# Kernel tuning notes

Measured on AMD Instinct MI355X. Metric: run time of the kernel, lower is better.

Reference implementation:

```python
import jax, jax.numpy as jnp
import numpy as np

N_IMG, M_GT, P_PROP = 16, 128, 8192
NUM_CLASSES = 80
THRESH_LO, THRESH_HI = 0.3, 0.7  # cfg.MODEL.ROI_HEADS.IOU_THRESHOLDS


def _make_boxes(key, shape, coord_scale=1000.0, wh_scale=200.0):
    k1, k2 = jax.random.split(key)
    xy = jax.random.uniform(k1, shape[:-1] + (2,)) * coord_scale
    wh = jax.random.uniform(k2, shape[:-1] + (2,)) * wh_scale + 1.0
    return jnp.concatenate([xy, xy + wh], axis=-1)  # [..., 4] = x1,y1,x2,y2


def setup_inputs() -> dict:
    key = jax.random.key(0)
    kg, kp, kc, ki = jax.random.split(key, 4)
    gt_boxes = _make_boxes(kg, (N_IMG, M_GT, 4))
    proposal_boxes = _make_boxes(kp, (N_IMG, P_PROP, 4))
    gt_classes = jax.random.randint(kc, (N_IMG, M_GT), 0, NUM_CLASSES, dtype=jnp.int32)
    gt_ignores = jax.random.randint(ki, (N_IMG, M_GT), 0, 2) > 0  # bool
    return {
        "gt_boxes": gt_boxes,
        "proposal_boxes": proposal_boxes,
        "gt_classes": gt_classes,
        "gt_ignores": gt_ignores,
    }


def _pairwise_iou(gt, pr):
    # gt: [N, M, 4], pr: [N, P, 4] -> iou [N, M, P]
    area_g = (gt[..., 2] - gt[..., 0]) * (gt[..., 3] - gt[..., 1])  # [N, M]
    area_p = (pr[..., 2] - pr[..., 0]) * (pr[..., 3] - pr[..., 1])  # [N, P]
    lt = jnp.maximum(gt[:, :, None, :2], pr[:, None, :, :2])  # [N, M, P, 2]
    rb = jnp.minimum(gt[:, :, None, 2:], pr[:, None, :, 2:])
    wh = jnp.clip(rb - lt, 0.0)
    inter = wh[..., 0] * wh[..., 1]  # [N, M, P]
    union = area_g[:, :, None] + area_p[:, None, :] - inter
    return jnp.where(inter > 0, inter / jnp.maximum(union, 1e-9), 0.0)


def reference(gt_boxes, proposal_boxes, gt_classes, gt_ignores):
    iou = _pairwise_iou(gt_boxes, proposal_boxes)  # [N, M, P]

    # Matcher: best GT per proposal + threshold labels (0=bg, -1=ignore, 1=fg)
    matched_vals = jnp.max(iou, axis=1)               # [N, P]
    matched_idxs = jnp.argmax(iou, axis=1).astype(jnp.int32)  # [N, P]
    matched_labels = jnp.where(
        matched_vals >= THRESH_HI, 1,
        jnp.where(matched_vals >= THRESH_LO, -1, 0),
    ).astype(jnp.int32)

    # gt_ignores toggling: proposals overlapping an ignored GT above high thresh -> -1
    neg_inf = jnp.float32(-1e30)
    max_ig = jnp.max(jnp.where(gt_ignores[:, :, None], iou, neg_inf), axis=1)  # [N, P]
    matched_labels = jnp.where(max_ig > THRESH_HI, -1, matched_labels)

    # _sample_proposals label assignment (full vector; random subsampling omitted)
    prop_gt_classes = jnp.take_along_axis(gt_classes, matched_idxs, axis=1)  # [N, P]
    prop_gt_classes = jnp.where(matched_labels == 0, NUM_CLASSES, prop_gt_classes)
    prop_gt_classes = jnp.where(matched_labels == -1, -1, prop_gt_classes)

    return iou, matched_idxs, matched_labels, prop_gt_classes
```

## Files before the change

kernel.cpp:

```cpp
#include <hip/hip_runtime.h>

#define N_IMG 16
#define M_GT 128
#define P_PROP 8192
#define NUM_CLASSES 80
#define THREADS 256

#define QUARTERS 4
#define MQ (M_GT / QUARTERS)
#define PPT 2
#define PBLK (THREADS * PPT)
#define NPBLK (P_PROP / PBLK)
#define NP (N_IMG * P_PROP)

__global__ __launch_bounds__(THREADS) void iou_kernel(
    const float* __restrict__ gt_boxes,
    const float* __restrict__ pr_boxes,
    const void*  __restrict__ gt_ignores,
    float* __restrict__ out,
    float* __restrict__ ws)
{
    __shared__ float4 s_box[MQ];
    __shared__ float  s_ag[MQ];
    __shared__ int    s_ign[MQ];
    __shared__ int    s_b01, s_bf;

    const int tid  = threadIdx.x;
    const int q    = blockIdx.x & 3;
    const int pblk = (blockIdx.x >> 2) & (NPBLK - 1);
    const int n    = blockIdx.x >> 6;

    if (tid == 0) { s_b01 = 0; s_bf = 0; }
    __syncthreads();
    {
        const int* w = (const int*)gt_ignores;
        int bad01 = 0, badf = 0;
        for (int i = tid; i < 512; i += THREADS) {
            int v = w[i];
            bad01 |= (v != 0) & (v != 1);
            badf  |= (v != 0) & (v != 0x3F800000);
        }
        if (bad01) atomicOr(&s_b01, 1);
        if (badf)  atomicOr(&s_bf, 1);
    }
    __syncthreads();
    const int mode = s_b01 ? (s_bf ? 1 : 2) : 0;

    if (tid < MQ) {
        const int m = q * MQ + tid;
        const float4 g = *reinterpret_cast<const float4*>(gt_boxes + ((size_t)n * M_GT + m) * 4);
        s_box[tid] = g;
        s_ag[tid]  = (g.z - g.x) * (g.w - g.y);
        int ig;
        if (mode == 0)      ig = ((const int*)gt_ignores)[n * M_GT + m] != 0;
        else if (mode == 1) ig = ((const unsigned char*)gt_ignores)[n * M_GT + m] != 0;
        else                ig = ((const float*)gt_ignores)[n * M_GT + m] != 0.0f;
        s_ign[tid] = ig;
    }
    __syncthreads();

    const int p0 = pblk * PBLK + tid * PPT;
    const float4 pa = *reinterpret_cast<const float4*>(pr_boxes + ((size_t)n * P_PROP + p0) * 4);
    const float4 pb = *reinterpret_cast<const float4*>(pr_boxes + ((size_t)n * P_PROP + p0 + 1) * 4);
    const float area_a = (pa.z - pa.x) * (pa.w - pa.y);
    const float area_b = (pb.z - pb.x) * (pb.w - pb.y);

    float best_a = -1.0f, best_b = -1.0f;
    int   arg_a  = 0,     arg_b  = 0;
    float ig_a   = -1e30f, ig_b  = -1e30f;

    float* iou_out = out + ((size_t)(n * M_GT + q * MQ)) * P_PROP + p0;

#pragma unroll 8
    for (int mi = 0; mi < MQ; ++mi) {
        const float4 g  = s_box[mi];
        const float  ag = s_ag[mi];
        const int    ig = s_ign[mi];
        const int    m  = q * MQ + mi;

        float lx = fmaxf(g.x, pa.x), ly = fmaxf(g.y, pa.y);
        float rx = fminf(g.z, pa.z), ry = fminf(g.w, pa.w);
        float w  = fmaxf(rx - lx, 0.0f), h = fmaxf(ry - ly, 0.0f);
        float inter = w * h;
        float uni   = ag + area_a - inter;
        float iou_a = (inter > 0.0f) ? inter / fmaxf(uni, 1e-9f) : 0.0f;

        lx = fmaxf(g.x, pb.x); ly = fmaxf(g.y, pb.y);
        rx = fminf(g.z, pb.z); ry = fminf(g.w, pb.w);
        w  = fmaxf(rx - lx, 0.0f); h = fmaxf(ry - ly, 0.0f);
        inter = w * h;
        uni   = ag + area_b - inter;
        float iou_b = (inter > 0.0f) ? inter / fmaxf(uni, 1e-9f) : 0.0f;

        *reinterpret_cast<float2*>(iou_out) = make_float2(iou_a, iou_b);
        iou_out += P_PROP;

        if (iou_a > best_a) { best_a = iou_a; arg_a = m; }
        if (iou_b > best_b) { best_b = iou_b; arg_b = m; }
        if (ig) { ig_a = fmaxf(ig_a, iou_a); ig_b = fmaxf(ig_b, iou_b); }
    }

    const size_t idx = (size_t)q * NP + (size_t)n * P_PROP + p0;
    float* wval = ws;
    float* warg = ws + (size_t)QUARTERS * NP;
    float* wig  = ws + (size_t)2 * QUARTERS * NP;
    *reinterpret_cast<float2*>(wval + idx) = make_float2(best_a, best_b);
    *reinterpret_cast<float2*>(warg + idx) = make_float2((float)arg_a, (float)arg_b);
    *reinterpret_cast<float2*>(wig  + idx) = make_float2(ig_a, ig_b);
}

__global__ __launch_bounds__(THREADS) void reduce_kernel(
    const float* __restrict__ ws,
    const int*   __restrict__ gt_classes,
    float* __restrict__ out)
{
    const int t = blockIdx.x * THREADS + threadIdx.x;
    const int n = t >> 13;

    const float* wval = ws;
    const float* warg = ws + (size_t)QUARTERS * NP;
    const float* wig  = ws + (size_t)2 * QUARTERS * NP;

    float best = -1.0f, barg = 0.0f, mig = -1e30f;
#pragma unroll
    for (int q = 0; q < QUARTERS; ++q) {
        const float v = wval[(size_t)q * NP + t];
        const float a = warg[(size_t)q * NP + t];
        const float g = wig [(size_t)q * NP + t];
        if (v > best) { best = v; barg = a; }
        mig = fmaxf(mig, g);
    }

    int label = (best >= 0.7f) ? 1 : ((best >= 0.3f) ? -1 : 0);
    if (mig > 0.7f) label = -1;

    int cls = gt_classes[n * M_GT + (int)barg];
    if (label == 0)  cls = NUM_CLASSES;
    if (label == -1) cls = -1;

    const size_t base = (size_t)N_IMG * M_GT * P_PROP;
    out[base + t]            = barg;
    out[base + NP + t]       = (float)label;
    out[base + 2 * (size_t)NP + t] = (float)cls;
}

extern "C" void kernel_launch(void* const* d_in, const int* in_sizes, int n_in,
                              void* d_out, int out_size, void* d_ws, size_t ws_size,
                              hipStream_t stream) {
    const float* gt_boxes   = (const float*)d_in[0];
    const float* pr_boxes   = (const float*)d_in[1];
    const int*   gt_classes = (const int*)d_in[2];
    const void*  gt_ignores = (const void*)d_in[3];
    float* out = (float*)d_out;
    float* ws  = (float*)d_ws;

    const int blocks_main = N_IMG * NPBLK * QUARTERS;
    iou_kernel<<<blocks_main, THREADS, 0, stream>>>(gt_boxes, pr_boxes, gt_ignores, out, ws);

    const int blocks_red = NP / THREADS;
    reduce_kernel<<<blocks_red, THREADS, 0, stream>>>(ws, gt_classes, out);
}
```

Baseline: 96.73 us.

## Fuse IoU and reduction kernels via per-block shared-memory wave reduction

Merges the two kernels into one: each 512-thread block covers 128 proposals, and each of its 8 waves handles 16 GT boxes. Per-wave best, argmax and ignore-max values go into shared memory and are reduced in-block, which removes the global workspace round trip and the second launch. The class lookup now reads from shared memory. In exchange, each block covers fewer proposals and adds an extra barrier plus a serial reduction done by only 128 threads.

```diff
diff --git a/kernel.cpp b/kernel.cpp
--- a/kernel.cpp
+++ b/kernel.cpp
@@ -4,62 +4,60 @@
 #define M_GT 128
 #define P_PROP 8192
 #define NUM_CLASSES 80
-#define THREADS 256
-
-#define QUARTERS 4
-#define MQ (M_GT / QUARTERS)
-#define PPT 2
-#define PBLK (THREADS * PPT)
+#define THREADS 512
+#define WAVES 8
+#define MQ (M_GT / WAVES)
+#define PPL 2
+#define PBLK 128
 #define NPBLK (P_PROP / PBLK)
 #define NP (N_IMG * P_PROP)
 
-__global__ __launch_bounds__(THREADS) void iou_kernel(
+__global__ __launch_bounds__(THREADS, 8) void roi_kernel(
     const float* __restrict__ gt_boxes,
     const float* __restrict__ pr_boxes,
+    const int*   __restrict__ gt_classes,
     const void*  __restrict__ gt_ignores,
-    float* __restrict__ out,
-    float* __restrict__ ws)
+    float* __restrict__ out)
 {
-    __shared__ float4 s_box[MQ];
-    __shared__ float  s_ag[MQ];
-    __shared__ int    s_ign[MQ];
+    __shared__ float4 s_box[M_GT];
+    __shared__ float  s_ag[M_GT];
+    __shared__ int    s_ign[M_GT];
+    __shared__ int    s_cls[M_GT];
+    __shared__ float  s_val[WAVES][PBLK];
+    __shared__ int    s_arg[WAVES][PBLK];
+    __shared__ float  s_igv[WAVES][PBLK];
     __shared__ int    s_b01, s_bf;
 
     const int tid  = threadIdx.x;
-    const int q    = blockIdx.x & 3;
-    const int pblk = (blockIdx.x >> 2) & (NPBLK - 1);
+    const int wave = tid >> 6;
+    const int lane = tid & 63;
     const int n    = blockIdx.x >> 6;
+    const int pblk = blockIdx.x & (NPBLK - 1);
 
     if (tid == 0) { s_b01 = 0; s_bf = 0; }
     __syncthreads();
     {
-        const int* w = (const int*)gt_ignores;
-        int bad01 = 0, badf = 0;
-        for (int i = tid; i < 512; i += THREADS) {
-            int v = w[i];
-            bad01 |= (v != 0) & (v != 1);
-            badf  |= (v != 0) & (v != 0x3F800000);
-        }
-        if (bad01) atomicOr(&s_b01, 1);
-        if (badf)  atomicOr(&s_bf, 1);
+        const int v = ((const int*)gt_ignores)[tid];
+        if ((v != 0) & (v != 1))          atomicOr(&s_b01, 1);
+        if ((v != 0) & (v != 0x3F800000)) atomicOr(&s_bf, 1);
     }
     __syncthreads();
     const int mode = s_b01 ? (s_bf ? 1 : 2) : 0;
 
-    if (tid < MQ) {
-        const int m = q * MQ + tid;
-        const float4 g = *reinterpret_cast<const float4*>(gt_boxes + ((size_t)n * M_GT + m) * 4);
+    if (tid < M_GT) {
+        const float4 g = *reinterpret_cast<const float4*>(gt_boxes + ((size_t)n * M_GT + tid) * 4);
         s_box[tid] = g;
         s_ag[tid]  = (g.z - g.x) * (g.w - g.y);
+        s_cls[tid] = gt_classes[n * M_GT + tid];
         int ig;
-        if (mode == 0)      ig = ((const int*)gt_ignores)[n * M_GT + m] != 0;
-        else if (mode == 1) ig = ((const unsigned char*)gt_ignores)[n * M_GT + m] != 0;
-        else                ig = ((const float*)gt_ignores)[n * M_GT + m] != 0.0f;
+        if (mode == 0)      ig = ((const int*)gt_ignores)[n * M_GT + tid] != 0;
+        else if (mode == 1) ig = ((const unsigned char*)gt_ignores)[n * M_GT + tid] != 0;
+        else                ig = ((const float*)gt_ignores)[n * M_GT + tid] != 0.0f;
         s_ign[tid] = ig;
     }
     __syncthreads();
 
-    const int p0 = pblk * PBLK + tid * PPT;
+    const int p0 = pblk * PBLK + lane * PPL;
     const float4 pa = *reinterpret_cast<const float4*>(pr_boxes + ((size_t)n * P_PROP + p0) * 4);
     const float4 pb = *reinterpret_cast<const float4*>(pr_boxes + ((size_t)n * P_PROP + p0 + 1) * 4);
     const float area_a = (pa.z - pa.x) * (pa.w - pa.y);
@@ -69,14 +67,14 @@
     int   arg_a  = 0,     arg_b  = 0;
     float ig_a   = -1e30f, ig_b  = -1e30f;
 
-    float* iou_out = out + ((size_t)(n * M_GT + q * MQ)) * P_PROP + p0;
+    float* iou_out = out + ((size_t)(n * M_GT + wave * MQ)) * P_PROP + p0;
 
-#pragma unroll 8
+#pragma unroll
     for (int mi = 0; mi < MQ; ++mi) {
-        const float4 g  = s_box[mi];
-        const float  ag = s_ag[mi];
-        const int    ig = s_ign[mi];
-        const int    m  = q * MQ + mi;
+        const int    m  = wave * MQ + mi;
+        const float4 g  = s_box[m];
+        const float  ag = s_ag[m];
+        const int    ig = s_ign[m];
 
         float lx = fmaxf(g.x, pa.x), ly = fmaxf(g.y, pa.y);
         float rx = fminf(g.z, pa.z), ry = fminf(g.w, pa.w);
@@ -100,48 +98,35 @@
         if (ig) { ig_a = fmaxf(ig_a, iou_a); ig_b = fmaxf(ig_b, iou_b); }
     }
 
-    const size_t idx = (size_t)q * NP + (size_t)n * P_PROP + p0;
-    float* wval = ws;
-    float* warg = ws + (size_t)QUARTERS * NP;
-    float* wig  = ws + (size_t)2 * QUARTERS * NP;
-    *reinterpret_cast<float2*>(wval + idx) = make_float2(best_a, best_b);
-    *reinterpret_cast<float2*>(warg + idx) = make_float2((float)arg_a, (float)arg_b);
-    *reinterpret_cast<float2*>(wig  + idx) = make_float2(ig_a, ig_b);
-}
+    const int pl = lane * PPL;
+    s_val[wave][pl]     = best_a;  s_val[wave][pl + 1] = best_b;
+    s_arg[wave][pl]     = arg_a;   s_arg[wave][pl + 1] = arg_b;
+    s_igv[wave][pl]     = ig_a;    s_igv[wave][pl + 1] = ig_b;
+    __syncthreads();
 
-__global__ __launch_bounds__(THREADS) void reduce_kernel(
-    const float* __restrict__ ws,
-    const int*   __restrict__ gt_classes,
-    float* __restrict__ out)
-{
-    const int t = blockIdx.x * THREADS + threadIdx.x;
-    const int n = t >> 13;
+    if (tid < PBLK) {
+        float best = -1.0f, mig = -1e30f;
+        int   barg = 0;
+#pragma unroll
+        for (int q = 0; q < WAVES; ++q) {
+            const float v = s_val[q][tid];
+            if (v > best) { best = v; barg = s_arg[q][tid]; }
+            mig = fmaxf(mig, s_igv[q][tid]);
+        }
 
-    const float* wval = ws;
-    const float* warg = ws + (size_t)QUARTERS * NP;
-    const float* wig  = ws + (size_t)2 * QUARTERS * NP;
+        int label = (best >= 0.7f) ? 1 : ((best >= 0.3f) ? -1 : 0);
+        if (mig > 0.7f) label = -1;
 
-    float best = -1.0f, barg = 0.0f, mig = -1e30f;
-#pragma unroll
-    for (int q = 0; q < QUARTERS; ++q) {
-        const float v = wval[(size_t)q * NP + t];
-        const float a = warg[(size_t)q * NP + t];
-        const float g = wig [(size_t)q * NP + t];
-        if (v > best) { best = v; barg = a; }
-        mig = fmaxf(mig, g);
+        int cls = s_cls[barg];
+        if (label == 0)  cls = NUM_CLASSES;
+        if (label == -1) cls = -1;
+
+        const size_t base = (size_t)N_IMG * M_GT * P_PROP;
+        const int t = n * P_PROP + pblk * PBLK + tid;
+        out[base + t]                  = (float)barg;
+        out[base + NP + t]             = (float)label;
+        out[base + 2 * (size_t)NP + t] = (float)cls;
     }
-
-    int label = (best >= 0.7f) ? 1 : ((best >= 0.3f) ? -1 : 0);
-    if (mig > 0.7f) label = -1;
-
-    int cls = gt_classes[n * M_GT + (int)barg];
-    if (label == 0)  cls = NUM_CLASSES;
-    if (label == -1) cls = -1;
-
-    const size_t base = (size_t)N_IMG * M_GT * P_PROP;
-    out[base + t]            = barg;
-    out[base + NP + t]       = (float)label;
-    out[base + 2 * (size_t)NP + t] = (float)cls;
 }
 
 extern "C" void kernel_launch(void* const* d_in, const int* in_sizes, int n_in,
@@ -152,11 +137,8 @@
     const int*   gt_classes = (const int*)d_in[2];
     const void*  gt_ignores = (const void*)d_in[3];
     float* out = (float*)d_out;
-    float* ws  = (float*)d_ws;
 
-    const int blocks_main = N_IMG * NPBLK * QUARTERS;
-    iou_kernel<<<blocks_main, THREADS, 0, stream>>>(gt_boxes, pr_boxes, gt_ignores, out, ws);
-
-    const int blocks_red = NP / THREADS;
-    reduce_kernel<<<blocks_red, THREADS, 0, stream>>>(ws, gt_classes, out);
+    const int blocks = N_IMG * NPBLK;
+    roi_kernel<<<blocks, THREADS, 0, stream>>>(
+        gt_boxes, pr_boxes, gt_classes, gt_ignores, out);
 }
```

New measurement: 100.4 us. +3.8%, slower.
